# Optimization experiments

Measured on AMD Instinct MI355X. Metric: run time of the kernel, lower is better.

Reference implementation:

```python
import jax, jax.numpy as jnp
import numpy as np
import math

B, S, D, H, HD, M, E = 4, 1024, 1024, 16, 64, 4096, 1024
EPS = 1e-6

def rms_norm(x, w):
    # torch: x / (||x||/sqrt(d) + eps) * w  (eps added to the norm, not norm^2)
    n = jnp.sqrt(jnp.sum(x * x, axis=-1, keepdims=True)) / math.sqrt(x.shape[-1])
    return x / (n + EPS) * w

def rope(x):
    # x: (B,H,S,hd)
    hd, s = x.shape[-1], x.shape[2]
    inv = 1.0 / (10000.0 ** (jnp.arange(0, hd, 2, dtype=jnp.float32) / hd))
    fr = jnp.arange(s, dtype=jnp.float32)[:, None] * inv[None, :]        # (S, hd/2)
    emb = jnp.concatenate([fr, fr], axis=-1)                              # (S, hd)
    cos, sin = jnp.cos(emb), jnp.sin(emb)
    x1, x2 = x[..., : hd // 2], x[..., hd // 2 :]
    rot = jnp.concatenate([-x2, x1], axis=-1)
    return x * cos + rot * sin

def setup_inputs() -> dict:
    key = jax.random.key(0)
    ks = jax.random.split(key, 18)
    p = lambda k, sh: jax.random.normal(k, sh, jnp.float32) * 0.02
    return {
        'x': jax.random.normal(ks[0], (B, S, D), jnp.float32),
        'emb': jax.random.normal(ks[1], (B, E), jnp.float32),
        'ln1_w': jnp.ones((D,), jnp.float32),
        'ln1_lW': p(ks[2], (E, 2 * D)), 'ln1_lb': p(ks[3], (2 * D,)),
        'ln2_w': jnp.ones((D,), jnp.float32),
        'ln2_lW': p(ks[4], (E, 2 * D)), 'ln2_lb': p(ks[5], (2 * D,)),
        'qkv_W': p(ks[6], (D, 3 * D)), 'qkv_b': p(ks[7], (3 * D,)),
        'proj_W': p(ks[8], (D, D)), 'proj_b': p(ks[9], (D,)),
        'nq_w': jnp.ones((HD,), jnp.float32), 'nk_w': jnp.ones((HD,), jnp.float32),
        'mlp_W': p(ks[10], (D, 2 * M)), 'mlp_b': p(ks[11], (2 * M,)),
        'out_W': p(ks[12], (M, D)), 'out_b': p(ks[13], (D,)),
        'gates_W': p(ks[14], (E, 2 * D)), 'gates_b': p(ks[15], (2 * D,)),
    }

def reference(x, emb, ln1_w, ln1_lW, ln1_lb, ln2_w, ln2_lW, ln2_lb,
              qkv_W, qkv_b, proj_W, proj_b, nq_w, nk_w,
              mlp_W, mlp_b, out_W, out_b, gates_W, gates_b):
    g = emb @ gates_W + gates_b                       # (B, 2D)
    gate_mha, gate_mlp = g[:, :D], g[:, D:]
    # AdaLNZero 1
    ss = emb @ ln1_lW + ln1_lb                        # (B, 2D): [scale | shift]
    xn = rms_norm(x, ln1_w) * (1.0 + ss[:, None, :D]) + ss[:, None, D:]
    # RoPE attention with qk RMSNorm
    qkv = (xn @ qkv_W + qkv_b).reshape(B, S, 3, H, HD).transpose(2, 0, 3, 1, 4)
    q, k, v = qkv[0], qkv[1], qkv[2]                  # each (B,H,S,HD)
    q = rms_norm(rope(q), nq_w)
    k = rms_norm(rope(k), nk_w)
    scores = jnp.einsum('bhqd,bhkd->bhqk', q, k) * (HD ** -0.5)
    attn = jnp.nan_to_num(jax.nn.softmax(scores, axis=-1))
    ao = jnp.einsum('bhqk,bhkd->bhqd', attn, v).transpose(0, 2, 1, 3).reshape(B, S, D)
    x = x + gate_mha[:, None, :] * (ao @ proj_W + proj_b)
    # AdaLNZero 2 + SwiGLU MLP
    ss2 = emb @ ln2_lW + ln2_lb
    xn2 = rms_norm(x, ln2_w) * (1.0 + ss2[:, None, :D]) + ss2[:, None, D:]
    h = xn2 @ mlp_W + mlp_b                           # (B,S,2M)
    act = h[..., :M] * jax.nn.silu(h[..., M:])
    mlp_out = act @ out_W + out_b
    return x + gate_mlp[:, None, :] * mlp_out
```

## Files before the change

kernel.cpp:

```cpp
#include <hip/hip_runtime.h>
#include <hip/hip_bf16.h>
#include <math.h>

#define B_ 4
#define S_ 1024
#define D_ 1024
#define H_ 16
#define HD_ 64
#define M_ 4096
#define E_ 1024

using bf16 = __hip_bfloat16;
typedef short bf16x8 __attribute__((ext_vector_type(8)));
typedef float f32x4 __attribute__((ext_vector_type(4)));

__device__ __forceinline__ void gl_lds16(const void* g, void* l) {
    __builtin_amdgcn_global_load_lds(
        (__attribute__((address_space(1))) void*)(g),
        (__attribute__((address_space(3))) void*)(l), 16, 0, 0);
}



#define STG_A(q, pb, kc) gl_lds16(A  + gAoff[q] + (kc), &sA[pb][(q) * 4096 + tid * 8])
#define STG_B(q, pb, kc) gl_lds16(Bt + gBoff[q] + (kc), &sB[pb][(q) * 4096 + tid * 8])

#define LDA(mh, m, h) (*(const bf16x8*)(cA + aRow + (mh) * 8192 + (m) * 2048 + (h)))
#define LDB(nh, n, h) (*(const bf16x8*)(cB + bRow + (nh) * 4096 + (n) * 2048 + (h)))

#define MFMA_QUAD(MH, NH, BF)                                                             \
    __builtin_amdgcn_s_setprio(1);                                                        \
    _Pragma("unroll")                                                                     \
    for (int m = 0; m < 4; ++m) {                                                         \
        _Pragma("unroll")                                                                 \
        for (int n = 0; n < 2; ++n) {                                                     \
            acc[(MH)*4+m][(NH)*2+n] = __builtin_amdgcn_mfma_f32_16x16x32_bf16(            \
                aF[m][0], BF[n][0], acc[(MH)*4+m][(NH)*2+n], 0, 0, 0);                    \
            acc[(MH)*4+m][(NH)*2+n] = __builtin_amdgcn_mfma_f32_16x16x32_bf16(            \
                aF[m][1], BF[n][1], acc[(MH)*4+m][(NH)*2+n], 0, 0, 0);                    \
        }                                                                                 \
    }                                                                                     \
    __builtin_amdgcn_s_setprio(0);

#define GEMM256_LOOP                                                                      \
    const int nt = K >> 6;                                                                \
    for (int t = 0; t < nt; ++t) {                                                        \
        const int pb = t & 1;                                                             \
        const char* cA = (const char*)sA[pb];                                             \
        const char* cB = (const char*)sB[pb];                                             \
        const int kc2 = (t + 2) << 6;                                                     \
        const bool pf = (t + 2) < nt;                                                     \
        bf16x8 aF[4][2], b0F[2][2], b1F[2][2];                                            \
                                          \
        _Pragma("unroll")                                                                 \
        for (int m = 0; m < 4; ++m) {                                                     \
            aF[m][0] = LDA(0, m, cs0);                                                    \
            aF[m][1] = LDA(0, m, cs1);                                                    \
        }                                                                                 \
        _Pragma("unroll")                                                                 \
        for (int n = 0; n < 2; ++n) {                                                     \
            b0F[n][0] = LDB(0, n, cs0);                                                   \
            b0F[n][1] = LDB(0, n, cs1);                                                   \
        }                                                                                 \
        __builtin_amdgcn_s_barrier();                                                     \
        asm volatile("s_waitcnt lgkmcnt(0)" ::: "memory");                                \
        MFMA_QUAD(0, 0, b0F)                                                              \
        __builtin_amdgcn_s_barrier();                                                     \
                         \
        _Pragma("unroll")                                                                 \
        for (int n = 0; n < 2; ++n) {                                                     \
            b1F[n][0] = LDB(1, n, cs0);                                                   \
            b1F[n][1] = LDB(1, n, cs1);                                                   \
        }                                                                                 \
        if (pf) { STG_A(0, pb, kc2); STG_A(2, pb, kc2); }                                 \
        __builtin_amdgcn_s_barrier();                                                     \
        asm volatile("s_waitcnt lgkmcnt(0)" ::: "memory");                                \
        MFMA_QUAD(0, 1, b1F)                                                              \
        __builtin_amdgcn_s_barrier();                                                     \
                               \
        _Pragma("unroll")                                                                 \
        for (int m = 0; m < 4; ++m) {                                                     \
            aF[m][0] = LDA(1, m, cs0);                                                    \
            aF[m][1] = LDA(1, m, cs1);                                                    \
        }                                                                                 \
        if (pf) { STG_B(0, pb, kc2); STG_B(1, pb, kc2);                                   \
                  STG_B(2, pb, kc2); STG_B(3, pb, kc2); }                                 \
        __builtin_amdgcn_s_barrier();                                                     \
        asm volatile("s_waitcnt lgkmcnt(0)" ::: "memory");                                \
        MFMA_QUAD(1, 1, b1F)                                                              \
        __builtin_amdgcn_s_barrier();                                                     \
                                 \
        if (pf) { STG_A(1, pb, kc2); STG_A(3, pb, kc2); }                                 \
        __builtin_amdgcn_s_barrier();                                                     \
        asm volatile("s_waitcnt lgkmcnt(0)" ::: "memory");                                \
        MFMA_QUAD(1, 0, b0F)                                                              \
        if (pf)              { asm volatile("s_waitcnt vmcnt(8)" ::: "memory"); }         \
        else if (t + 1 < nt) { asm volatile("s_waitcnt vmcnt(0)" ::: "memory"); }         \
        __builtin_amdgcn_s_barrier();                                                     \
    }

__global__ __launch_bounds__(256) void transpose_kernel(
    const float* __restrict__ W, bf16* __restrict__ Wt, int K, int N)
{
    __shared__ float tile[32][33];
    int n0 = blockIdx.x * 32, k0 = blockIdx.y * 32;
    int tx = threadIdx.x & 31, ty = threadIdx.x >> 5;
    #pragma unroll
    for (int r = ty; r < 32; r += 8)
        tile[r][tx] = W[(long)(k0 + r) * N + n0 + tx];
    __syncthreads();
    #pragma unroll
    for (int r = ty; r < 32; r += 8)
        Wt[(long)(n0 + r) * K + k0 + tx] = __float2bfloat16(tile[tx][r]);
}

__global__ __launch_bounds__(256) void embgemm_kernel(
    const float* __restrict__ emb,
    const float* __restrict__ W0, const float* __restrict__ b0,
    const float* __restrict__ W1, const float* __restrict__ b1,
    const float* __restrict__ W2, const float* __restrict__ b2,
    float* __restrict__ G, float* __restrict__ SS, float* __restrict__ SS2)
{
    __shared__ float se[256];
    int b = blockIdx.y;
    int k0 = blockIdx.z * 256;
    if (threadIdx.x < 256) se[threadIdx.x] = emb[b * 1024 + k0 + threadIdx.x];
    __syncthreads();
    int j = blockIdx.x * 256 + threadIdx.x;
    int which = j >> 11, col = j & 2047;
    const float* W  = which == 0 ? W0 : (which == 1 ? W1 : W2);
    const float* bb = which == 0 ? b0 : (which == 1 ? b1 : b2);
    float acc = (k0 == 0) ? bb[col] : 0.f;
    #pragma unroll 4
    for (int k = 0; k < 256; ++k) acc += se[k] * W[(long)(k0 + k) * 2048 + col];
    float* out = which == 0 ? G : (which == 1 ? SS : SS2);
    atomicAdd(&out[b * 2048 + col], acc);
}

__global__ __launch_bounds__(256) void rmsmod_kernel(
    const float* __restrict__ x, const float* __restrict__ w,
    const float* __restrict__ ss, bf16* __restrict__ out)
{
    int row = blockIdx.x;
    int b = row >> 10;
    const float* xr = x + (long)row * D_;
    float4 v = ((const float4*)xr)[threadIdx.x];
    float ssum = v.x * v.x + v.y * v.y + v.z * v.z + v.w * v.w;
    #pragma unroll
    for (int off = 32; off; off >>= 1) ssum += __shfl_xor(ssum, off);
    __shared__ float red[4];
    if ((threadIdx.x & 63) == 0) red[threadIdx.x >> 6] = ssum;
    __syncthreads();
    float tot = red[0] + red[1] + red[2] + red[3];
    float n = sqrtf(tot) * (1.f / 32.f);
    float inv = 1.f / (n + 1e-6f);
    int d0 = threadIdx.x * 4;
    const float* ssb = ss + b * 2048;
    bf16 t[4];
    t[0] = __float2bfloat16(v.x * inv * w[d0 + 0] * (1.f + ssb[d0 + 0]) + ssb[D_ + d0 + 0]);
    t[1] = __float2bfloat16(v.y * inv * w[d0 + 1] * (1.f + ssb[d0 + 1]) + ssb[D_ + d0 + 1]);
    t[2] = __float2bfloat16(v.z * inv * w[d0 + 2] * (1.f + ssb[d0 + 2]) + ssb[D_ + d0 + 2]);
    t[3] = __float2bfloat16(v.w * inv * w[d0 + 3] * (1.f + ssb[d0 + 3]) + ssb[D_ + d0 + 3]);
    *(uint2*)&out[(long)row * D_ + d0] = *(uint2*)t;
}

__global__ __launch_bounds__(512) void gemm256_kernel(
    const bf16* __restrict__ A, const bf16* __restrict__ Bt,
    const float* __restrict__ bias, bf16* __restrict__ Cb,
    int N, int K)
{
    __shared__ bf16 sA[2][16384];
    __shared__ bf16 sB[2][16384];
    const int tid = threadIdx.x;
    const int wave = tid >> 6, lane = tid & 63;
    const int wr = wave >> 2, wc = wave & 3;
    const int cl = lane & 15, qd = lane >> 4;

    const int num_pid_n = N >> 8;
    const int cpx = gridDim.x >> 3;
    int wg = (blockIdx.x & 7) * cpx + (blockIdx.x >> 3);
    const int group_size = 8 * num_pid_n;
    const int group_id = wg / group_size;
    const int pid_in = wg - group_id * group_size;
    const int m0 = (group_id * 8 + (pid_in & 7)) * 256;
    const int n0 = (pid_in >> 3) * 256;

    long gAoff[4], gBoff[4];
    #pragma unroll
    for (int q = 0; q < 4; ++q) {
        int c = tid + q * 512;
        int cs = c ^ ((c >> 3) & 7);
        int row = cs >> 3, col = (cs & 7) * 8;
        gAoff[q] = (long)(m0 + row) * K + col;
        gBoff[q] = (long)(n0 + row) * K + col;
    }

    #pragma unroll
    for (int q = 0; q < 4; ++q) { STG_A(q, 0, 0); STG_B(q, 0, 0); }
    #pragma unroll
    for (int q = 0; q < 4; ++q) { STG_A(q, 1, 64); STG_B(q, 1, 64); }

    f32x4 acc[8][4] = {};
    const int swz = (cl & 7) << 4;
    const int aRow = (wr * 128 + cl) * 128;
    const int bRow = (wc * 64 + cl) * 128;
    const int cs0 = (qd * 16) ^ swz;
    const int cs1 = (qd * 16 + 64) ^ swz;

    asm volatile("s_waitcnt vmcnt(8)" ::: "memory");
    __builtin_amdgcn_s_barrier();

    GEMM256_LOOP

    #pragma unroll
    for (int m = 0; m < 8; ++m) {
        #pragma unroll
        for (int n = 0; n < 4; ++n) {
            int col = n0 + wc * 64 + n * 16 + cl;
            float bs = bias[col];
            #pragma unroll
            for (int i = 0; i < 4; ++i) {
                int row = m0 + wr * 128 + m * 16 + qd * 4 + i;
                Cb[(long)row * N + col] = __float2bfloat16(acc[m][n][i] + bs);
            }
        }
    }
}

__global__ __launch_bounds__(512) void gemm256_mlp_kernel(
    const bf16* __restrict__ A, const bf16* __restrict__ Bt,
    const float* __restrict__ bias, bf16* __restrict__ ACT, int K)
{
    __shared__ bf16 sA[2][16384];
    __shared__ bf16 sB[2][16384];
    const int tid = threadIdx.x;
    const int wave = tid >> 6, lane = tid & 63;
    const int wr = wave >> 2, wc = wave & 3;
    const int cl = lane & 15, qd = lane >> 4;

    const int num_pid_n = 32;
    const int cpx = gridDim.x >> 3;
    int wg = (blockIdx.x & 7) * cpx + (blockIdx.x >> 3);
    const int group_size = 8 * num_pid_n;
    const int group_id = wg / group_size;
    const int pid_in = wg - group_id * group_size;
    const int m0 = (group_id * 8 + (pid_in & 7)) * 256;
    const int n0 = (pid_in >> 3) * 128;

    long gAoff[4], gBoff[4];
    #pragma unroll
    for (int q = 0; q < 4; ++q) {
        int c = tid + q * 512;
        int cs = c ^ ((c >> 3) & 7);
        int row = cs >> 3, col = (cs & 7) * 8;
        gAoff[q] = (long)(m0 + row) * K + col;
        int pp = row >> 5, hf = (row >> 4) & 1, wi = row & 15;
        gBoff[q] = (long)(hf * 4096 + n0 + pp * 16 + wi) * K + col;
    }

    #pragma unroll
    for (int q = 0; q < 4; ++q) { STG_A(q, 0, 0); STG_B(q, 0, 0); }
    #pragma unroll
    for (int q = 0; q < 4; ++q) { STG_A(q, 1, 64); STG_B(q, 1, 64); }

    f32x4 acc[8][4] = {};
    const int swz = (cl & 7) << 4;
    const int aRow = (wr * 128 + cl) * 128;
    const int bRow = (wc * 64 + cl) * 128;
    const int cs0 = (qd * 16) ^ swz;
    const int cs1 = (qd * 16 + 64) ^ swz;

    asm volatile("s_waitcnt vmcnt(8)" ::: "memory");
    __builtin_amdgcn_s_barrier();

    GEMM256_LOOP

    #pragma unroll
    for (int m = 0; m < 8; ++m) {
        #pragma unroll
        for (int pr = 0; pr < 2; ++pr) {
            int col = n0 + wc * 32 + pr * 16 + cl;
            float bs1 = bias[col];
            float bs2 = bias[4096 + col];
            #pragma unroll
            for (int i = 0; i < 4; ++i) {
                int row = m0 + wr * 128 + m * 16 + qd * 4 + i;
                float h1 = acc[m][pr * 2 + 0][i] + bs1;
                float h2 = acc[m][pr * 2 + 1][i] + bs2;
                float sg = 1.f / (1.f + __expf(-h2));
                ACT[(long)row * 4096 + col] = __float2bfloat16(h1 * h2 * sg);
            }
        }
    }
}

#define MFMA_HQ(MH)                                                                       \
    __builtin_amdgcn_s_setprio(1);                                                        \
    _Pragma("unroll")                                                                     \
    for (int m = 0; m < 4; ++m) {                                                         \
        _Pragma("unroll")                                                                 \
        for (int n = 0; n < 2; ++n) {                                                     \
            acc[(MH)*4+m][n] = __builtin_amdgcn_mfma_f32_16x16x32_bf16(                   \
                aF[m][0], bF[n][0], acc[(MH)*4+m][n], 0, 0, 0);                           \
            acc[(MH)*4+m][n] = __builtin_amdgcn_mfma_f32_16x16x32_bf16(                   \
                aF[m][1], bF[n][1], acc[(MH)*4+m][n], 0, 0, 0);                           \
        }                                                                                 \
    }                                                                                     \
    __builtin_amdgcn_s_setprio(0);

__global__ __launch_bounds__(512) void gemm256x128_kernel(
    const bf16* __restrict__ A, const bf16* __restrict__ Bt,
    float* __restrict__ P0, float* __restrict__ P1, int N, int K)
{
    __shared__ bf16 sA[2][16384];
    __shared__ bf16 sB[2][8192];
    const int tid = threadIdx.x;
    const int wave = tid >> 6, lane = tid & 63;
    const int wr = wave >> 2, wc = wave & 3;
    const int cl = lane & 15, qd = lane >> 4;

    const int cpx = gridDim.x >> 3;
    int wg = (blockIdx.x & 7) * cpx + (blockIdx.x >> 3);
    const int split = wg >> 7;
    const int w2 = wg & 127;
    const int group_id = w2 >> 6;
    const int pid_in = w2 & 63;
    const int m0 = (group_id * 8 + (pid_in & 7)) * 256;
    const int n0 = (pid_in >> 3) * 128;
    const int Kh = K >> 1;
    A  += (long)split * Kh;
    Bt += (long)split * Kh;

    long gAoff[4], gBoff[2];
    #pragma unroll
    for (int q = 0; q < 4; ++q) {
        int c = tid + q * 512;
        int cs = c ^ ((c >> 3) & 7);
        int row = cs >> 3, col = (cs & 7) * 8;
        gAoff[q] = (long)(m0 + row) * K + col;
        if (q < 2) gBoff[q] = (long)(n0 + row) * K + col;
    }

    const int nt = Kh >> 6;
    STG_A(0, 0, 0); STG_A(2, 0, 0); STG_B(0, 0, 0); STG_B(1, 0, 0);
    STG_A(1, 0, 0); STG_A(3, 0, 0);
    if (nt > 1) { STG_A(0, 1, 64); STG_A(2, 1, 64); STG_B(0, 1, 64); STG_B(1, 1, 64); }

    f32x4 acc[8][2] = {};
    const int swz = (cl & 7) << 4;
    const int aRow = (wr * 128 + cl) * 128;
    const int bRow = (wc * 32 + cl) * 128;
    const int cs0 = (qd * 16) ^ swz;
    const int cs1 = (qd * 16 + 64) ^ swz;

    if (nt > 1) { asm volatile("s_waitcnt vmcnt(4)" ::: "memory"); }
    else        { asm volatile("s_waitcnt vmcnt(0)" ::: "memory"); }
    __builtin_amdgcn_s_barrier();

    for (int t = 0; t < nt; ++t) {
        const int pb = t & 1;
        const char* cA = (const char*)sA[pb];
        const char* cB = (const char*)sB[pb];
        bf16x8 aF[4][2], bF[2][2];
        #pragma unroll
        for (int m = 0; m < 4; ++m) {
            aF[m][0] = *(const bf16x8*)(cA + aRow + m * 2048 + cs0);
            aF[m][1] = *(const bf16x8*)(cA + aRow + m * 2048 + cs1);
        }
        #pragma unroll
        for (int n = 0; n < 2; ++n) {
            bF[n][0] = *(const bf16x8*)(cB + bRow + n * 2048 + cs0);
            bF[n][1] = *(const bf16x8*)(cB + bRow + n * 2048 + cs1);
        }
        if (t + 1 < nt) { STG_A(1, pb ^ 1, (t + 1) << 6); STG_A(3, pb ^ 1, (t + 1) << 6); }
        __builtin_amdgcn_s_barrier();
        asm volatile("s_waitcnt lgkmcnt(0)" ::: "memory");
        MFMA_HQ(0)
        __builtin_amdgcn_s_barrier();
        #pragma unroll
        for (int m = 0; m < 4; ++m) {
            aF[m][0] = *(const bf16x8*)(cA + aRow + 8192 + m * 2048 + cs0);
            aF[m][1] = *(const bf16x8*)(cA + aRow + 8192 + m * 2048 + cs1);
        }
        if (t + 2 < nt) { STG_A(0, pb, (t + 2) << 6); STG_A(2, pb, (t + 2) << 6);
                          STG_B(0, pb, (t + 2) << 6); STG_B(1, pb, (t + 2) << 6); }
        __builtin_amdgcn_s_barrier();
        asm volatile("s_waitcnt lgkmcnt(0)" ::: "memory");
        MFMA_HQ(1)
        if (t + 2 < nt)      { asm volatile("s_waitcnt vmcnt(4)" ::: "memory"); }
        else if (t + 1 < nt) { asm volatile("s_waitcnt vmcnt(0)" ::: "memory"); }
        __builtin_amdgcn_s_barrier();
    }

    float* P = split ? P1 : P0;
    #pragma unroll
    for (int m = 0; m < 8; ++m) {
        #pragma unroll
        for (int n = 0; n < 2; ++n) {
            int col = n0 + wc * 32 + n * 16 + cl;
            #pragma unroll
            for (int i = 0; i < 4; ++i) {
                int row = m0 + wr * 128 + m * 16 + qd * 4 + i;
                P[(long)row * N + col] = acc[m][n][i];
            }
        }
    }
}

__global__ __launch_bounds__(256) void fuseout_kernel(
    const float* __restrict__ p0, const float* __restrict__ p1,
    const float* __restrict__ bias, const float* __restrict__ resid,
    const float* __restrict__ gates, float* __restrict__ out)
{
    int idx = blockIdx.x * 256 + threadIdx.x;
    int row = idx >> 8;
    int b = row >> 10;
    int c4 = (idx & 255) * 4;
    float4 a = ((const float4*)p0)[idx];
    float4 c = ((const float4*)p1)[idx];
    float4 r = ((const float4*)resid)[idx];
    float4 bb = *(const float4*)&bias[c4];
    float4 gg = *(const float4*)&gates[b * 2048 + 1024 + c4];
    float4 o;
    o.x = r.x + gg.x * (a.x + c.x + bb.x);
    o.y = r.y + gg.y * (a.y + c.y + bb.y);
    o.z = r.z + gg.z * (a.z + c.z + bb.z);
    o.w = r.w + gg.w * (a.w + c.w + bb.w);
    ((float4*)out)[idx] = o;
}

__global__ __launch_bounds__(256) void gemm64_kernel(
    const bf16* __restrict__ A, const bf16* __restrict__ Bt,
    const float* __restrict__ bias,
    bf16* __restrict__ Cb, float* __restrict__ Cf,
    const float* __restrict__ resid, const float* __restrict__ gates, int gate_off,
    int Mrows, int N, int K, int mode)
{
    __shared__ bf16 sA[64 * 32];
    __shared__ bf16 sB[64 * 32];
    const int tid = threadIdx.x;
    const int wave = tid >> 6, lane = tid & 63;
    const int num_pid_n = N >> 6;
    const int pid = blockIdx.x;
    const int group_size = 8 * num_pid_n;
    const int group_id = pid / group_size;
    const int pid_in = pid - group_id * group_size;
    const int pid_m = group_id * 8 + (pid_in & 7);
    const int pid_n = pid_in >> 3;
    const int m0 = pid_m * 64, n0 = pid_n * 64;
    const int wm = (wave & 1) * 32, wn = (wave >> 1) * 32;
    const int cl = lane & 15, qd = lane >> 4;

    f32x4 acc[2][2] = {};

    const int c = tid;
    const int rr = c >> 2, ss = (c & 3) ^ ((c >> 3) & 3);
    const bf16* gA = A + (long)(m0 + rr) * K + ss * 8;
    const bf16* gB = Bt + (long)(n0 + rr) * K + ss * 8;
    bf16* lA = &sA[wave * 512];
    bf16* lB = &sB[wave * 512];

    const int q8s = (qd ^ ((cl >> 1) & 3)) * 8;

    for (int kc = 0; kc < K; kc += 32) {
        gl_lds16(gA + kc, lA);
        gl_lds16(gB + kc, lB);
        __syncthreads();
        bf16x8 af[2], bfr[2];
        #pragma unroll
        for (int t = 0; t < 2; ++t)
            af[t] = *(const bf16x8*)&sA[(wm + cl + t * 16) * 32 + q8s];
        #pragma unroll
        for (int u = 0; u < 2; ++u)
            bfr[u] = *(const bf16x8*)&sB[(wn + cl + u * 16) * 32 + q8s];
        #pragma unroll
        for (int t = 0; t < 2; ++t)
            #pragma unroll
            for (int u = 0; u < 2; ++u)
                acc[t][u] = __builtin_amdgcn_mfma_f32_16x16x32_bf16(af[t], bfr[u], acc[t][u], 0, 0, 0);
        __syncthreads();
    }

    #pragma unroll
    for (int t = 0; t < 2; ++t) {
        #pragma unroll
        for (int u = 0; u < 2; ++u) {
            int col = n0 + wn + u * 16 + cl;
            float bs = bias[col];
            #pragma unroll
            for (int i = 0; i < 4; ++i) {
                int row = m0 + wm + t * 16 + qd * 4 + i;
                float v = acc[t][u][i] + bs;
                if (mode == 0) {
                    Cb[(long)row * N + col] = __float2bfloat16(v);
                } else {
                    int b = row >> 10;
                    float g = gates[b * 2048 + gate_off + col];
                    Cf[(long)row * N + col] = resid[(long)row * N + col] + g * v;
                }
            }
        }
    }
}

__global__ __launch_bounds__(256) void ropenorm_kernel(
    const bf16* __restrict__ qkv, const float* __restrict__ nq_w, const float* __restrict__ nk_w,
    bf16* __restrict__ qh, bf16* __restrict__ kh, bf16* __restrict__ vt)
{
    int gid = blockIdx.x * 4 + (threadIdx.x >> 6);
    int lane = threadIdx.x & 63;
    int b = gid >> 14, s = (gid >> 4) & (S_ - 1), h = gid & (H_ - 1);
    const long base = (long)(b * S_ + s) * 3072 + h * 64 + lane;
    float qv = __bfloat162float(qkv[base]);
    float kv = __bfloat162float(qkv[base + 1024]);
    float vv = __bfloat162float(qkv[base + 2048]);
    int j = lane & 31;
    float inv = exp2f(-(float)j * (13.287712379549449f / 32.f));
    float ang = (float)s * inv;
    float sn, c;
    sincosf(ang, &sn, &c);
    float pq = __shfl_xor(qv, 32);
    float pk = __shfl_xor(kv, 32);
    float rq = (lane < 32) ? -pq : pq;
    float rk = (lane < 32) ? -pk : pk;
    float qr = qv * c + rq * sn;
    float kr = kv * c + rk * sn;
    float sq = qr * qr, sk = kr * kr;
    #pragma unroll
    for (int off = 32; off; off >>= 1) { sq += __shfl_xor(sq, off); sk += __shfl_xor(sk, off); }
    float nq = sqrtf(sq) * 0.125f;
    float nk = sqrtf(sk) * 0.125f;
    float qo = qr / (nq + 1e-6f) * nq_w[lane];
    float ko = kr / (nk + 1e-6f) * nk_w[lane];
    long hb = ((long)(b * H_ + h) * S_ + s) * 64 + lane;
    qh[hb] = __float2bfloat16(qo);
    kh[hb] = __float2bfloat16(ko);
    vt[((long)(b * H_ + h) * 64 + lane) * S_ + s] = __float2bfloat16(vv);
}

__global__ __launch_bounds__(256) void attn_kernel(
    const bf16* __restrict__ qh, const bf16* __restrict__ kh, const bf16* __restrict__ vt,
    bf16* __restrict__ ao)
{
    const int bh = blockIdx.y;
    const int q0 = blockIdx.x * 64;
    const int tid = threadIdx.x, wave = tid >> 6, lane = tid & 63;
    const int cl = lane & 15, qd = lane >> 4;

    __shared__ bf16 sQ[64 * 72];
    __shared__ bf16 sK[64 * 72];
    __shared__ bf16 sV[64 * 72];
    __shared__ bf16 sP[4][16 * 72];

    {
        const bf16* Qg = qh + (long)bh * S_ * 64 + (long)q0 * 64;
        int a = tid, b2 = tid + 256;
        *(uint4*)&sQ[(a >> 3) * 72 + (a & 7) * 8]  = *(const uint4*)&Qg[(a >> 3) * 64 + (a & 7) * 8];
        *(uint4*)&sQ[(b2 >> 3) * 72 + (b2 & 7) * 8] = *(const uint4*)&Qg[(b2 >> 3) * 64 + (b2 & 7) * 8];
    }

    float l_i[4] = {0.f, 0.f, 0.f, 0.f};
    f32x4 o_acc[4] = {};

    const bf16* Kg = kh + (long)bh * S_ * 64;
    const bf16* Vg = vt + (long)bh * 64 * S_;

    for (int kv0 = 0; kv0 < S_; kv0 += 64) {
        __syncthreads();
        {
            int a = tid, b2 = tid + 256;
            *(uint4*)&sK[(a >> 3) * 72 + (a & 7) * 8]   = *(const uint4*)&Kg[((long)kv0 + (a >> 3)) * 64 + (a & 7) * 8];
            *(uint4*)&sK[(b2 >> 3) * 72 + (b2 & 7) * 8] = *(const uint4*)&Kg[((long)kv0 + (b2 >> 3)) * 64 + (b2 & 7) * 8];
            *(uint4*)&sV[(a >> 3) * 72 + (a & 7) * 8]   = *(const uint4*)&Vg[(long)(a >> 3) * S_ + kv0 + (a & 7) * 8];
            *(uint4*)&sV[(b2 >> 3) * 72 + (b2 & 7) * 8] = *(const uint4*)&Vg[(long)(b2 >> 3) * S_ + kv0 + (b2 & 7) * 8];
        }
        __syncthreads();

        f32x4 sfr[4] = {};
        #pragma unroll
        for (int u = 0; u < 4; ++u) {
            #pragma unroll
            for (int ks = 0; ks < 2; ++ks) {
                bf16x8 aq = *(const bf16x8*)&sQ[(wave * 16 + cl) * 72 + ks * 32 + qd * 8];
                bf16x8 bk = *(const bf16x8*)&sK[(u * 16 + cl) * 72 + ks * 32 + qd * 8];
                sfr[u] = __builtin_amdgcn_mfma_f32_16x16x32_bf16(aq, bk, sfr[u], 0, 0, 0);
            }
        }

        #pragma unroll
        for (int i = 0; i < 4; ++i) {
            float sum = 0.f;
            #pragma unroll
            for (int u = 0; u < 4; ++u) {
                float p = __expf(sfr[u][i] * 0.125f - 8.f);
                sum += p;
                sP[wave][(qd * 4 + i) * 72 + u * 16 + cl] = __float2bfloat16(p);
            }
            sum += __shfl_xor(sum, 1);
            sum += __shfl_xor(sum, 2);
            sum += __shfl_xor(sum, 4);
            sum += __shfl_xor(sum, 8);
            l_i[i] += sum;
        }

        #pragma unroll
        for (int ks = 0; ks < 2; ++ks) {
            bf16x8 ap = *(const bf16x8*)&sP[wave][cl * 72 + ks * 32 + qd * 8];
            #pragma unroll
            for (int u = 0; u < 4; ++u) {
                bf16x8 bv = *(const bf16x8*)&sV[(u * 16 + cl) * 72 + ks * 32 + qd * 8];
                o_acc[u] = __builtin_amdgcn_mfma_f32_16x16x32_bf16(ap, bv, o_acc[u], 0, 0, 0);
            }
        }
    }

    #pragma unroll
    for (int i = 0; i < 4; ++i) {
        float invl = 1.f / l_i[i];
        int row = q0 + wave * 16 + qd * 4 + i;
        #pragma unroll
        for (int u = 0; u < 4; ++u) {
            int d = u * 16 + cl;
            ao[((long)(bh >> 4) * S_ + row) * D_ + (bh & 15) * 64 + d] =
                __float2bfloat16(o_acc[u][i] * invl);
        }
    }
}

extern "C" void kernel_launch(void* const* d_in, const int* in_sizes, int n_in,
                              void* d_out, int out_size, void* d_ws, size_t ws_size,
                              hipStream_t stream) {
    const float* x       = (const float*)d_in[0];
    const float* emb     = (const float*)d_in[1];
    const float* ln1_w   = (const float*)d_in[2];
    const float* ln1_lW  = (const float*)d_in[3];
    const float* ln1_lb  = (const float*)d_in[4];
    const float* ln2_w   = (const float*)d_in[5];
    const float* ln2_lW  = (const float*)d_in[6];
    const float* ln2_lb  = (const float*)d_in[7];
    const float* qkv_W   = (const float*)d_in[8];
    const float* qkv_b   = (const float*)d_in[9];
    const float* proj_W  = (const float*)d_in[10];
    const float* proj_b  = (const float*)d_in[11];
    const float* nq_w    = (const float*)d_in[12];
    const float* nk_w    = (const float*)d_in[13];
    const float* mlp_W   = (const float*)d_in[14];
    const float* mlp_b   = (const float*)d_in[15];
    const float* out_W   = (const float*)d_in[16];
    const float* out_b   = (const float*)d_in[17];
    const float* gates_W = (const float*)d_in[18];
    const float* gates_b = (const float*)d_in[19];
    float* out = (float*)d_out;

    char* p = (char*)d_ws;
    if (ws_size < 159481856UL) return;
    bf16* WT_QKV  = (bf16*)p;  p += 6291456;
    bf16* WT_PROJ = (bf16*)p;  p += 2097152;
    bf16* WT_MLP  = (bf16*)p;  p += 16777216;
    bf16* WT_OUT  = (bf16*)p;  p += 8388608;
    float* G      = (float*)p; p += 32768;
    float* SSb    = (float*)p; p += 32768;
    float* SS2b   = (float*)p; p += 32768;
    float* X1     = (float*)p; p += 16777216;
    bf16* XN2     = (bf16*)p;  p += 8388608;
    bf16* ACT     = (bf16*)p;  p += 33554432;
    char* REG = p;
    bf16* XN   = (bf16*)(REG);
    bf16* QKV  = (bf16*)(REG + 8388608);
    bf16* QH   = (bf16*)(REG + 33554432);
    bf16* KH   = (bf16*)(REG + 41943040);
    bf16* VT   = (bf16*)(REG + 50331648);
    bf16* AO   = (bf16*)(REG + 58720256);
    float* PF0 = (float*)(REG);
    float* PF1 = (float*)(REG + 16777216);

    dim3 blk(256);
    hipMemsetAsync(G, 0, 98304, stream);
    transpose_kernel<<<dim3(96, 32),  blk, 0, stream>>>(qkv_W,  WT_QKV, 1024, 3072);
    transpose_kernel<<<dim3(32, 32),  blk, 0, stream>>>(proj_W, WT_PROJ, 1024, 1024);
    transpose_kernel<<<dim3(256, 32), blk, 0, stream>>>(mlp_W,  WT_MLP, 1024, 8192);
    transpose_kernel<<<dim3(32, 128), blk, 0, stream>>>(out_W,  WT_OUT, 4096, 1024);
    embgemm_kernel<<<dim3(24, 4, 4), blk, 0, stream>>>(emb, gates_W, gates_b, ln1_lW, ln1_lb,
                                                       ln2_lW, ln2_lb, G, SSb, SS2b);
    rmsmod_kernel<<<dim3(4096), blk, 0, stream>>>(x, ln1_w, SSb, XN);
    gemm256_kernel<<<dim3(192), dim3(512), 0, stream>>>(XN, WT_QKV, qkv_b, QKV, 3072, 1024);
    ropenorm_kernel<<<dim3(16384), blk, 0, stream>>>(QKV, nq_w, nk_w, QH, KH, VT);
    attn_kernel<<<dim3(16, 64), blk, 0, stream>>>(QH, KH, VT, AO);
    gemm64_kernel<<<dim3(1024), blk, 0, stream>>>(AO, WT_PROJ, proj_b, nullptr, X1,
                                                  x, G, 0, 4096, 1024, 1024, 1);
    rmsmod_kernel<<<dim3(4096), blk, 0, stream>>>(X1, ln2_w, SS2b, XN2);
    gemm256_mlp_kernel<<<dim3(512), dim3(512), 0, stream>>>(XN2, WT_MLP, mlp_b, ACT, 1024);
    gemm256x128_kernel<<<dim3(256), dim3(512), 0, stream>>>(ACT, WT_OUT, PF0, PF1, 1024, 4096);
    fuseout_kernel<<<dim3(4096), blk, 0, stream>>>(PF0, PF1, out_b, X1, G, out);
}
```

Baseline: 480.8 us.

## Fuse RoPE and QK RMSNorm into QKV GEMM epilogue; merge weight transposes

The QKV GEMM epilogue now applies bias, RoPE and per-head RMSNorm to Q and K directly from the accumulators, using shuffles across the 16-lane column group. It writes head-major Q/K and transposed V, which removes the separate ropenorm kernel and the round trip of the QKV intermediate through memory. The four weight transpose launches are also merged into one launch. The cost is more epilogue math (sincos per element) and scattered 2-byte stores for Q/K, which may coalesce poorly.

Result: slower. 491.4 us (+2.2%).

```diff
diff --git a/kernel.cpp b/kernel.cpp
--- a/kernel.cpp
+++ b/kernel.cpp
@@ -99,11 +99,34 @@
         __builtin_amdgcn_s_barrier();                                                     \
     }
 
-__global__ __launch_bounds__(256) void transpose_kernel(
-    const float* __restrict__ W, bf16* __restrict__ Wt, int K, int N)
+#define GEMM256_PROLOG(NPN, N0MUL)                                                        \
+    const int tid = threadIdx.x;                                                          \
+    const int wave = tid >> 6, lane = tid & 63;                                           \
+    const int wr = wave >> 2, wc = wave & 3;                                              \
+    const int cl = lane & 15, qd = lane >> 4;                                             \
+    const int num_pid_n = (NPN);                                                          \
+    const int cpx = gridDim.x >> 3;                                                       \
+    int wg = (blockIdx.x & 7) * cpx + (blockIdx.x >> 3);                                  \
+    const int group_size = 8 * num_pid_n;                                                 \
+    const int group_id = wg / group_size;                                                 \
+    const int pid_in = wg - group_id * group_size;                                        \
+    const int m0 = (group_id * 8 + (pid_in & 7)) * 256;                                   \
+    const int n0 = (pid_in >> 3) * (N0MUL);
+
+__global__ __launch_bounds__(256) void transpose_all_kernel(
+    const float* __restrict__ W0, bf16* __restrict__ T0,
+    const float* __restrict__ W1, bf16* __restrict__ T1,
+    const float* __restrict__ W2, bf16* __restrict__ T2,
+    const float* __restrict__ W3, bf16* __restrict__ T3)
 {
     __shared__ float tile[32][33];
-    int n0 = blockIdx.x * 32, k0 = blockIdx.y * 32;
+    int id = blockIdx.x;
+    const float* W; bf16* T; int K, N, bx, by;
+    if (id < 3072)       { W = W0; T = T0; K = 1024; N = 3072; bx = id % 96;  by = id / 96; }
+    else if (id < 4096)  { id -= 3072;  W = W1; T = T1; K = 1024; N = 1024; bx = id & 31;  by = id >> 5; }
+    else if (id < 12288) { id -= 4096;  W = W2; T = T2; K = 1024; N = 8192; bx = id & 255; by = id >> 8; }
+    else                 { id -= 12288; W = W3; T = T3; K = 4096; N = 1024; bx = id & 31;  by = id >> 5; }
+    int n0 = bx * 32, k0 = by * 32;
     int tx = threadIdx.x & 31, ty = threadIdx.x >> 5;
     #pragma unroll
     for (int r = ty; r < 32; r += 8)
@@ -111,7 +134,7 @@
     __syncthreads();
     #pragma unroll
     for (int r = ty; r < 32; r += 8)
-        Wt[(long)(n0 + r) * K + k0 + tx] = __float2bfloat16(tile[tx][r]);
+        T[(long)(n0 + r) * K + k0 + tx] = __float2bfloat16(tile[tx][r]);
 }
 
 __global__ __launch_bounds__(256) void embgemm_kernel(
@@ -164,26 +187,16 @@
     *(uint2*)&out[(long)row * D_ + d0] = *(uint2*)t;
 }
 
-__global__ __launch_bounds__(512) void gemm256_kernel(
+__global__ __launch_bounds__(512) void qkvgemm_kernel(
     const bf16* __restrict__ A, const bf16* __restrict__ Bt,
-    const float* __restrict__ bias, bf16* __restrict__ Cb,
+    const float* __restrict__ bias,
+    const float* __restrict__ nq_w, const float* __restrict__ nk_w,
+    bf16* __restrict__ qh, bf16* __restrict__ kh, bf16* __restrict__ vt,
     int N, int K)
 {
     __shared__ bf16 sA[2][16384];
     __shared__ bf16 sB[2][16384];
-    const int tid = threadIdx.x;
-    const int wave = tid >> 6, lane = tid & 63;
-    const int wr = wave >> 2, wc = wave & 3;
-    const int cl = lane & 15, qd = lane >> 4;
-
-    const int num_pid_n = N >> 8;
-    const int cpx = gridDim.x >> 3;
-    int wg = (blockIdx.x & 7) * cpx + (blockIdx.x >> 3);
-    const int group_size = 8 * num_pid_n;
-    const int group_id = wg / group_size;
-    const int pid_in = wg - group_id * group_size;
-    const int m0 = (group_id * 8 + (pid_in & 7)) * 256;
-    const int n0 = (pid_in >> 3) * 256;
+    GEMM256_PROLOG(N >> 8, 256)
 
     long gAoff[4], gBoff[4];
     #pragma unroll
@@ -212,16 +225,62 @@
 
     GEMM256_LOOP
 
-    #pragma unroll
-    for (int m = 0; m < 8; ++m) {
+    const int third = n0 >> 10;
+    const int h = ((n0 & 1023) >> 6) + wc;
+    const int b = m0 >> 10;
+    const int s0 = (m0 & 1023) + wr * 128;
+    const int colb = n0 + wc * 64;
+    float bs0 = bias[colb + cl],      bs1 = bias[colb + 16 + cl];
+    float bs2 = bias[colb + 32 + cl], bs3 = bias[colb + 48 + cl];
+
+    if (third == 2) {
         #pragma unroll
         for (int n = 0; n < 4; ++n) {
-            int col = n0 + wc * 64 + n * 16 + cl;
-            float bs = bias[col];
+            int d = n * 16 + cl;
+            float bs = bias[colb + n * 16 + cl];
+            long rowd = ((long)(b * 16 + h) * 64 + d) * 1024;
+            #pragma unroll
+            for (int m = 0; m < 8; ++m) {
+                int sb = s0 + m * 16 + qd * 4;
+                bf16 t4[4];
+                #pragma unroll
+                for (int i = 0; i < 4; ++i)
+                    t4[i] = __float2bfloat16(acc[m][n][i] + bs);
+                *(uint2*)&vt[rowd + sb] = *(uint2*)t4;
+            }
+        }
+    } else {
+        const float* w = (third == 0) ? nq_w : nk_w;
+        bf16* dst = (third == 0) ? qh : kh;
+        float inv0 = exp2f(-(float)cl        * (13.287712379549449f / 32.f));
+        float inv1 = exp2f(-(float)(16 + cl) * (13.287712379549449f / 32.f));
+        float w0 = w[cl], w1 = w[16 + cl], w2 = w[32 + cl], w3 = w[48 + cl];
+        long hb = ((long)(b * 16 + h) * 1024) * 64;
+        #pragma unroll
+        for (int m = 0; m < 8; ++m) {
             #pragma unroll
             for (int i = 0; i < 4; ++i) {
-                int row = m0 + wr * 128 + m * 16 + qd * 4 + i;
-                Cb[(long)row * N + col] = __float2bfloat16(acc[m][n][i] + bs);
+                int s = s0 + m * 16 + qd * 4 + i;
+                float v0 = acc[m][0][i] + bs0, v1 = acc[m][1][i] + bs1;
+                float v2 = acc[m][2][i] + bs2, v3 = acc[m][3][i] + bs3;
+                float sn0, c0, sn1, c1;
+                sincosf((float)s * inv0, &sn0, &c0);
+                sincosf((float)s * inv1, &sn1, &c1);
+                float r0 = v0 * c0 - v2 * sn0;
+                float r1 = v1 * c1 - v3 * sn1;
+                float r2 = v2 * c0 + v0 * sn0;
+                float r3 = v3 * c1 + v1 * sn1;
+                float ssq = r0 * r0 + r1 * r1 + r2 * r2 + r3 * r3;
+                ssq += __shfl_xor(ssq, 1);
+                ssq += __shfl_xor(ssq, 2);
+                ssq += __shfl_xor(ssq, 4);
+                ssq += __shfl_xor(ssq, 8);
+                float innv = 1.f / (sqrtf(ssq) * 0.125f + 1e-6f);
+                long ro = hb + (long)s * 64;
+                dst[ro + cl]      = __float2bfloat16(r0 * innv * w0);
+                dst[ro + 16 + cl] = __float2bfloat16(r1 * innv * w1);
+                dst[ro + 32 + cl] = __float2bfloat16(r2 * innv * w2);
+                dst[ro + 48 + cl] = __float2bfloat16(r3 * innv * w3);
             }
         }
     }
@@ -233,19 +292,7 @@
 {
     __shared__ bf16 sA[2][16384];
     __shared__ bf16 sB[2][16384];
-    const int tid = threadIdx.x;
-    const int wave = tid >> 6, lane = tid & 63;
-    const int wr = wave >> 2, wc = wave & 3;
-    const int cl = lane & 15, qd = lane >> 4;
-
-    const int num_pid_n = 32;
-    const int cpx = gridDim.x >> 3;
-    int wg = (blockIdx.x & 7) * cpx + (blockIdx.x >> 3);
-    const int group_size = 8 * num_pid_n;
-    const int group_id = wg / group_size;
-    const int pid_in = wg - group_id * group_size;
-    const int m0 = (group_id * 8 + (pid_in & 7)) * 256;
-    const int n0 = (pid_in >> 3) * 128;
+    GEMM256_PROLOG(32, 128)
 
     long gAoff[4], gBoff[4];
     #pragma unroll
@@ -501,41 +548,6 @@
             }
         }
     }
-}
-
-__global__ __launch_bounds__(256) void ropenorm_kernel(
-    const bf16* __restrict__ qkv, const float* __restrict__ nq_w, const float* __restrict__ nk_w,
-    bf16* __restrict__ qh, bf16* __restrict__ kh, bf16* __restrict__ vt)
-{
-    int gid = blockIdx.x * 4 + (threadIdx.x >> 6);
-    int lane = threadIdx.x & 63;
-    int b = gid >> 14, s = (gid >> 4) & (S_ - 1), h = gid & (H_ - 1);
-    const long base = (long)(b * S_ + s) * 3072 + h * 64 + lane;
-    float qv = __bfloat162float(qkv[base]);
-    float kv = __bfloat162float(qkv[base + 1024]);
-    float vv = __bfloat162float(qkv[base + 2048]);
-    int j = lane & 31;
-    float inv = exp2f(-(float)j * (13.287712379549449f / 32.f));
-    float ang = (float)s * inv;
-    float sn, c;
-    sincosf(ang, &sn, &c);
-    float pq = __shfl_xor(qv, 32);
-    float pk = __shfl_xor(kv, 32);
-    float rq = (lane < 32) ? -pq : pq;
-    float rk = (lane < 32) ? -pk : pk;
-    float qr = qv * c + rq * sn;
-    float kr = kv * c + rk * sn;
-    float sq = qr * qr, sk = kr * kr;
-    #pragma unroll
-    for (int off = 32; off; off >>= 1) { sq += __shfl_xor(sq, off); sk += __shfl_xor(sk, off); }
-    float nq = sqrtf(sq) * 0.125f;
-    float nk = sqrtf(sk) * 0.125f;
-    float qo = qr / (nq + 1e-6f) * nq_w[lane];
-    float ko = kr / (nk + 1e-6f) * nk_w[lane];
-    long hb = ((long)(b * H_ + h) * S_ + s) * 64 + lane;
-    qh[hb] = __float2bfloat16(qo);
-    kh[hb] = __float2bfloat16(ko);
-    vt[((long)(b * H_ + h) * 64 + lane) * S_ + s] = __float2bfloat16(vv);
 }
 
 __global__ __launch_bounds__(256) void attn_kernel(
@@ -666,7 +678,6 @@
     bf16* ACT     = (bf16*)p;  p += 33554432;
     char* REG = p;
     bf16* XN   = (bf16*)(REG);
-    bf16* QKV  = (bf16*)(REG + 8388608);
     bf16* QH   = (bf16*)(REG + 33554432);
     bf16* KH   = (bf16*)(REG + 41943040);
     bf16* VT   = (bf16*)(REG + 50331648);
@@ -676,15 +687,13 @@
 
     dim3 blk(256);
     hipMemsetAsync(G, 0, 98304, stream);
-    transpose_kernel<<<dim3(96, 32),  blk, 0, stream>>>(qkv_W,  WT_QKV, 1024, 3072);
-    transpose_kernel<<<dim3(32, 32),  blk, 0, stream>>>(proj_W, WT_PROJ, 1024, 1024);
-    transpose_kernel<<<dim3(256, 32), blk, 0, stream>>>(mlp_W,  WT_MLP, 1024, 8192);
-    transpose_kernel<<<dim3(32, 128), blk, 0, stream>>>(out_W,  WT_OUT, 4096, 1024);
+    transpose_all_kernel<<<dim3(16384), blk, 0, stream>>>(qkv_W, WT_QKV, proj_W, WT_PROJ,
+                                                          mlp_W, WT_MLP, out_W, WT_OUT);
     embgemm_kernel<<<dim3(24, 4, 4), blk, 0, stream>>>(emb, gates_W, gates_b, ln1_lW, ln1_lb,
                                                        ln2_lW, ln2_lb, G, SSb, SS2b);
     rmsmod_kernel<<<dim3(4096), blk, 0, stream>>>(x, ln1_w, SSb, XN);
-    gemm256_kernel<<<dim3(192), dim3(512), 0, stream>>>(XN, WT_QKV, qkv_b, QKV, 3072, 1024);
-    ropenorm_kernel<<<dim3(16384), blk, 0, stream>>>(QKV, nq_w, nk_w, QH, KH, VT);
+    qkvgemm_kernel<<<dim3(192), dim3(512), 0, stream>>>(XN, WT_QKV, qkv_b, nq_w, nk_w,
+                                                        QH, KH, VT, 3072, 1024);
     attn_kernel<<<dim3(16, 64), blk, 0, stream>>>(QH, KH, VT, AO);
     gemm64_kernel<<<dim3(1024), blk, 0, stream>>>(AO, WT_PROJ, proj_b, nullptr, X1,
                                                   x, G, 0, 4096, 1024, 1024, 1);
```
